# Performance work log

Hardware: AMD Instinct MI355X
Metric: run time of the kernel (lower is better)

## Reference

```python
import jax, jax.numpy as jnp
import numpy as np

T, B, N_IN, N_OUT = 100, 32, 1024, 512
LR_LTP, LR_LTD = 1e-4, -1e-4
TAU_PRE, TAU_POST, DT = 20.0, 20.0, 1.0
W_MIN, W_MAX = 0.0, 1.0
SPIKE_PROB = 0.05


def setup_inputs() -> dict:
    key = jax.random.key(0)
    k1, k2, k3 = jax.random.split(key, 3)
    weight = jax.random.uniform(k1, (N_OUT, N_IN), dtype=jnp.float32)
    pre_spikes = (jax.random.uniform(k2, (T, B, N_IN)) < SPIKE_PROB).astype(jnp.float32)
    post_spikes = (jax.random.uniform(k3, (T, B, N_OUT)) < SPIKE_PROB).astype(jnp.float32)
    pre_trace = jnp.zeros((B, N_IN), jnp.float32)
    post_trace = jnp.zeros((B, N_OUT), jnp.float32)
    return {"weight": weight, "pre_spikes": pre_spikes, "post_spikes": post_spikes,
            "pre_trace": pre_trace, "post_trace": post_trace}


def reference(weight, pre_spikes, post_spikes, pre_trace, post_trace):
    # weight: [N_out, N_in]; pre_spikes: [T,B,N_in]; post_spikes: [T,B,N_out]
    decay_pre = jnp.exp(jnp.asarray(-DT / TAU_PRE, weight.dtype))
    decay_post = jnp.exp(jnp.asarray(-DT / TAU_POST, weight.dtype))
    # Soft bounds (w_max=1.0 > 0 -> w_max - w; w_min=0.0 not < 0 -> w)
    soft_ltp = W_MAX - weight
    soft_ltd = weight
    Bf = jnp.asarray(pre_spikes.shape[1], weight.dtype)

    def step(carry, xs):
        pre_tr, post_tr, dw = carry
        pre_s, post_s = xs  # [B,N_in], [B,N_out]
        pre_tr = pre_tr * decay_pre + pre_s
        post_tr = post_tr * decay_post + post_s
        # batch-mean of outer products -> [N_out, N_in]
        ltp_mean = jnp.einsum('bo,bi->oi', post_s, pre_tr) / Bf
        ltd_mean = jnp.einsum('bo,bi->oi', post_tr, pre_s) / Bf
        dw = dw + LR_LTP * soft_ltp * ltp_mean + LR_LTD * soft_ltd * ltd_mean
        return (pre_tr, post_tr, dw), None

    init = (pre_trace, post_trace, jnp.zeros_like(weight))
    (pre_tr, post_tr, delta_w), _ = jax.lax.scan(step, init, (pre_spikes, post_spikes))
    return delta_w, pre_tr, post_tr
```

## Files before the change

kernel.cpp:

```cpp
#include <hip/hip_runtime.h>

typedef unsigned short ushort;
typedef unsigned int uint;
typedef unsigned char uchar;
typedef __attribute__((ext_vector_type(8))) int intx8;
typedef __attribute__((ext_vector_type(16))) float floatx16;

#define T_STEPS 100
#define BATCH   32
#define NIN     1024
#define NOUT    512

#define SEG      112
#define KPAD     (BATCH * SEG)
#define KSTRIDEB 3648

#define LR_LTP  (1e-4f)
#define LR_LTD  (-1e-4f)
#define INV_B   (1.0f / 32.0f)
#define DECAY   0.951229424500714f
#define D28     0.246596963941607f
#define TCH     28
#define NCHUNK  4

#define OFF_PRE  (NOUT * NIN)
#define OFF_POST (OFF_PRE + BATCH * NIN)

#define B_PRST  0
#define B_PRTT  ((size_t)NIN * KSTRIDEB)
#define B_POST  ((size_t)2 * NIN * KSTRIDEB)
#define B_POTT  ((size_t)2 * NIN * KSTRIDEB + (size_t)NOUT * KSTRIDEB)


static __device__ __forceinline__ uint pk4_fp8(float a, float b, float c, float d) {
    uint v = 0;
    v = __builtin_amdgcn_cvt_pk_fp8_f32(a, b, v, false);
    v = __builtin_amdgcn_cvt_pk_fp8_f32(c, d, v, true);
    return v;
}

static __device__ __forceinline__ intx8 ld32(const uchar* p) {
    const uint4 lo = *(const uint4*)p;
    const uint4 hv = *(const uint4*)(p + 16);
    intx8 r;
    r[0] = (int)lo.x; r[1] = (int)lo.y; r[2] = (int)lo.z; r[3] = (int)lo.w;
    r[4] = (int)hv.x; r[5] = (int)hv.y; r[6] = (int)hv.z; r[7] = (int)hv.w;
    return r;
}

__global__ __launch_bounds__(256) void stdp_traces_t(
    const float* __restrict__ pre_s,
    const float* __restrict__ post_s,
    const float* __restrict__ pre_tr0,
    const float* __restrict__ post_tr0,
    uchar* __restrict__ pre_s_t, uchar* __restrict__ pre_tr_t,
    uchar* __restrict__ post_s_t, uchar* __restrict__ post_tr_t,
    float* __restrict__ out)
{
    __shared__ uint Ls[64 * 33];
    __shared__ uint Lt[64 * 33];
    __shared__ float Eend[NCHUNK][64];

    const int chain = threadIdx.x & 63;
    const int c     = threadIdx.x >> 6;
    const int g     = blockIdx.x * 64 + chain;

    const float* src; const float* init;
    int id, stride, outoff;
    if (g < BATCH * NIN) {
        src = pre_s;  init = pre_tr0;
        id = g;               stride = BATCH * NIN;  outoff = OFF_PRE;
    } else {
        src = post_s; init = post_tr0;
        id = g - BATCH * NIN; stride = BATCH * NOUT; outoff = OFF_POST;
    }

    const int t0 = c * TCH;
    float x[TCH];
    #pragma unroll
    for (int m = 0; m < TCH; ++m)
        x[m] = (t0 + m < T_STEPS) ? src[(size_t)(t0 + m) * stride + id] : 0.f;

    uint sp[7];
    #pragma unroll
    for (int j = 0; j < 7; ++j)
        sp[j] = pk4_fp8(x[4*j], x[4*j+1], x[4*j+2], x[4*j+3]);

    float e = 0.f;
    #pragma unroll
    for (int m = 0; m < TCH; ++m) { e = e * DECAY + x[m]; x[m] = e; }
    Eend[c][chain] = e;
    __syncthreads();

    float C = init[id];
    for (int cc = 0; cc < c; ++cc) C = C * D28 + Eend[cc][chain];
    float p = C * DECAY;
    #pragma unroll
    for (int m = 0; m < TCH; ++m) { x[m] += p; p *= DECAY; }

    if (c == NCHUNK - 1) out[outoff + id] = x[15];

    #pragma unroll
    for (int j = 0; j < 7; ++j) {
        const uint tj = pk4_fp8(x[4*j], x[4*j+1], x[4*j+2], x[4*j+3]);
        Ls[chain * 33 + c * 7 + j] = sp[j];
        Lt[chain * 33 + c * 7 + j] = tj;
    }
    __syncthreads();

    const int id0 = blockIdx.x * 64;
    uchar *dS, *dT; int b0, ch0;
    if (id0 < BATCH * NIN) {
        b0 = id0 >> 10; ch0 = id0 & 1023; dS = pre_s_t;  dT = pre_tr_t;
    } else {
        const int idq = id0 - BATCH * NIN;
        b0 = idq >> 9;  ch0 = idq & 511;  dS = post_s_t; dT = post_tr_t;
    }
    #pragma unroll
    for (int j = 0; j < 4; ++j) {
        const int q = threadIdx.x + 256 * j;
        if (q < 896) {
            const int op = q >= 448;
            const int qq = q - op * 448;
            const int r  = qq / 7;
            const int cc = qq - r * 7;
            const uint* l = (op ? Lt : Ls) + r * 33 + cc * 4;
            const uint4 v = make_uint4(l[0], l[1], l[2], l[3]);
            uchar* gd = (op ? dT : dS) + (size_t)(ch0 + r) * KSTRIDEB + b0 * SEG + cc * 16;
            *(uint4*)gd = v;
        }
    }
}

__global__ __launch_bounds__(128) void stdp_gemm_dual(
    const uchar* __restrict__ post_s_t, const uchar* __restrict__ pre_tr_t,
    const uchar* __restrict__ post_tr_t, const uchar* __restrict__ pre_s_t,
    const float* __restrict__ wmat, float* __restrict__ out)
{
    const int i0 = blockIdx.x * 64;
    const int o0 = blockIdx.y * 32;

    const int tid  = threadIdx.x;
    const int wn   = tid >> 6;
    const int lane = tid & 63;
    const int l32  = lane & 31;
    const int hi   = lane >> 5;

    floatx16 accP, accD;
    #pragma unroll
    for (int r = 0; r < 16; ++r) { accP[r] = 0.f; accD[r] = 0.f; }

    const size_t aBase = (size_t)(o0 + l32) * KSTRIDEB + (hi << 5);
    const size_t bBase = (size_t)(i0 + wn * 32 + l32) * KSTRIDEB + (hi << 5);

    for (int kb = 0; kb < KPAD; kb += 64) {
        const intx8 aP = ld32(post_s_t  + aBase + kb);
        const intx8 aD = ld32(post_tr_t + aBase + kb);
        const intx8 bP = ld32(pre_tr_t  + bBase + kb);
        const intx8 bD = ld32(pre_s_t   + bBase + kb);
        accP = __builtin_amdgcn_mfma_scale_f32_32x32x64_f8f6f4(
            aP, bP, accP, 0, 0, 0, 127, 0, 127);
        accD = __builtin_amdgcn_mfma_scale_f32_32x32x64_f8f6f4(
            aD, bD, accD, 0, 0, 0, 127, 0, 127);
    }

    const float c1 = LR_LTP * INV_B;
    const float c2 = LR_LTD * INV_B;
    const int i  = i0 + wn * 32 + l32;
    const int ob = o0 + hi * 4;
    #pragma unroll
    for (int r = 0; r < 16; ++r) {
        const int o = ob + (r & 3) + 8 * (r >> 2);
        const size_t idx = (size_t)o * NIN + i;
        const float wv = wmat[idx];
        out[idx] = c1 * (1.0f - wv) * accP[r] + c2 * wv * accD[r];
    }
}

extern "C" void kernel_launch(void* const* d_in, const int* in_sizes, int n_in,
                              void* d_out, int out_size, void* d_ws, size_t ws_size,
                              hipStream_t stream) {
    const float* weight   = (const float*)d_in[0];
    const float* pre_s    = (const float*)d_in[1];
    const float* post_s   = (const float*)d_in[2];
    const float* pre_tr0  = (const float*)d_in[3];
    const float* post_tr0 = (const float*)d_in[4];
    float* out = (float*)d_out;

    uchar* wsb = (uchar*)d_ws;
    uchar* pre_s_t   = wsb + B_PRST;
    uchar* pre_tr_t  = wsb + B_PRTT;
    uchar* post_s_t  = wsb + B_POST;
    uchar* post_tr_t = wsb + B_POTT;

    stdp_traces_t<<<dim3(BATCH * (NIN + NOUT) / 64), dim3(256), 0, stream>>>(
        pre_s, post_s, pre_tr0, post_tr0,
        pre_s_t, pre_tr_t, post_s_t, post_tr_t, out);

    stdp_gemm_dual<<<dim3(NIN / 64, NOUT / 32), dim3(128), 0, stream>>>(
        post_s_t, pre_tr_t, post_tr_t, pre_s_t, weight, out);
}
```

Measured before the change: 104.4 us.

## Split GEMM K dimension across four waves with LDS reduction and XCD-aware tile mapping

```diff
diff --git a/kernel.cpp b/kernel.cpp
--- a/kernel.cpp
+++ b/kernel.cpp
@@ -14,6 +14,7 @@
 #define SEG      112
 #define KPAD     (BATCH * SEG)
 #define KSTRIDEB 3648
+#define KQ       (KPAD / 4)
 
 #define LR_LTP  (1e-4f)
 #define LR_LTD  (-1e-4f)
@@ -132,17 +133,23 @@
     }
 }
 
-__global__ __launch_bounds__(128) void stdp_gemm_dual(
+__global__ __launch_bounds__(256, 2) void stdp_gemm_dual(
     const uchar* __restrict__ post_s_t, const uchar* __restrict__ pre_tr_t,
     const uchar* __restrict__ post_tr_t, const uchar* __restrict__ pre_s_t,
     const float* __restrict__ wmat, float* __restrict__ out)
 {
-    const int i0 = blockIdx.x * 64;
-    const int o0 = blockIdx.y * 32;
-
-    const int tid  = threadIdx.x;
-    const int wn   = tid >> 6;
-    const int lane = tid & 63;
+    __shared__ float red[4][2][16][64];
+
+    const int bid = blockIdx.x;
+    const int xcd = bid & 7;
+    const int l   = bid >> 3;
+    const int ot  = (xcd & 1) * 8 + (l & 7);
+    const int it  = (xcd >> 1) * 8 + (l >> 3);
+    const int o0  = ot * 32;
+    const int i0  = it * 32;
+
+    const int w    = threadIdx.x >> 6;
+    const int lane = threadIdx.x & 63;
     const int l32  = lane & 31;
     const int hi   = lane >> 5;
 
@@ -151,9 +158,11 @@
     for (int r = 0; r < 16; ++r) { accP[r] = 0.f; accD[r] = 0.f; }
 
     const size_t aBase = (size_t)(o0 + l32) * KSTRIDEB + (hi << 5);
-    const size_t bBase = (size_t)(i0 + wn * 32 + l32) * KSTRIDEB + (hi << 5);
-
-    for (int kb = 0; kb < KPAD; kb += 64) {
+    const size_t bBase = (size_t)(i0 + l32) * KSTRIDEB + (hi << 5);
+    const int k0 = w * KQ;
+
+    #pragma unroll 2
+    for (int kb = k0; kb < k0 + KQ; kb += 64) {
         const intx8 aP = ld32(post_s_t  + aBase + kb);
         const intx8 aD = ld32(post_tr_t + aBase + kb);
         const intx8 bP = ld32(pre_tr_t  + bBase + kb);
@@ -164,16 +173,29 @@
             aD, bD, accD, 0, 0, 0, 127, 0, 127);
     }
 
+    #pragma unroll
+    for (int r = 0; r < 16; ++r) {
+        red[w][0][r][lane] = accP[r];
+        red[w][1][r][lane] = accD[r];
+    }
+    __syncthreads();
+
     const float c1 = LR_LTP * INV_B;
     const float c2 = LR_LTD * INV_B;
-    const int i  = i0 + wn * 32 + l32;
-    const int ob = o0 + hi * 4;
-    #pragma unroll
-    for (int r = 0; r < 16; ++r) {
-        const int o = ob + (r & 3) + 8 * (r >> 2);
+    #pragma unroll
+    for (int q = 0; q < 4; ++q) {
+        const int e  = threadIdx.x + 256 * q;
+        const int ln = e & 63;
+        const int r  = e >> 6;
+        const float sP = red[0][0][r][ln] + red[1][0][r][ln]
+                       + red[2][0][r][ln] + red[3][0][r][ln];
+        const float sD = red[0][1][r][ln] + red[1][1][r][ln]
+                       + red[2][1][r][ln] + red[3][1][r][ln];
+        const int o = o0 + (r & 3) + 8 * (r >> 2) + 4 * (ln >> 5);
+        const int i = i0 + (ln & 31);
         const size_t idx = (size_t)o * NIN + i;
         const float wv = wmat[idx];
-        out[idx] = c1 * (1.0f - wv) * accP[r] + c2 * wv * accD[r];
+        out[idx] = c1 * (1.0f - wv) * sP + c2 * wv * sD;
     }
 }
 
@@ -197,6 +219,6 @@
         pre_s, post_s, pre_tr0, post_tr0,
         pre_s_t, pre_tr_t, post_s_t, post_tr_t, out);
 
-    stdp_gemm_dual<<<dim3(NIN / 64, NOUT / 32), dim3(128), 0, stream>>>(
+    stdp_gemm_dual<<<dim3(512), dim3(256), 0, stream>>>(
         post_s_t, pre_tr_t, post_tr_t, pre_s_t, weight, out);
 }
```

Result: faster. 101.9 us (-2.3%).
